# Kernel optimization log

Measured on AMD Instinct MI355X. Metric: run time of the kernel, lower is better.

Reference implementation:

```python
import jax, jax.numpy as jnp
from jax import lax
import numpy as np

VOCAB = 100
EMBED = 16
STATE = 7
OUT = 10
B, T = 4096, 512


def setup_inputs() -> dict:
    key = jax.random.key(0)
    k0, k1, k2, k3, k4 = jax.random.split(key, 5)
    tokens = jax.random.randint(k0, (B, T), 0, VOCAB, dtype=jnp.int32)
    emb = jax.random.normal(k1, (VOCAB, EMBED), dtype=jnp.float32) * 0.05
    # LSTMCell params, Keras gate order: i, f, g(candidate), o
    W = jax.random.normal(k2, (EMBED, 4 * STATE), dtype=jnp.float32) * 0.1
    U = jax.random.normal(k3, (STATE, 4 * STATE), dtype=jnp.float32) * 0.1
    # unit_forget_bias=True in Keras: forget-gate bias initialized to 1
    b = jnp.concatenate([jnp.zeros(STATE), jnp.ones(STATE), jnp.zeros(2 * STATE)]).astype(jnp.float32)
    Wd = jax.random.normal(k4, (STATE, OUT), dtype=jnp.float32) * 0.1
    bd = jnp.zeros((OUT,), dtype=jnp.float32)
    return {"tokens": tokens, "emb": emb, "W": W, "U": U, "b": b, "Wd": Wd, "bd": bd}


def reference(tokens, emb, W, U, b, Wd, bd):
    x = emb[tokens]                      # [B, T, E] embedding lookup
    x_tm = jnp.swapaxes(x, 0, 1)         # [T, B, E] time-major for scan

    def step(carry, xt):
        h, c = carry                     # [B, S] each
        z = xt @ W + h @ U + b           # [B, 4S]
        zi, zf, zg, zo = jnp.split(z, 4, axis=-1)
        i = jax.nn.sigmoid(zi)
        f = jax.nn.sigmoid(zf)
        g = jnp.tanh(zg)
        o = jax.nn.sigmoid(zo)
        c_new = f * c + i * g
        h_new = o * jnp.tanh(c_new)
        return (h_new, c_new), h_new

    h0 = jnp.zeros((tokens.shape[0], STATE), dtype=x.dtype)
    c0 = jnp.zeros_like(h0)
    _, hs = lax.scan(step, (h0, c0), x_tm)   # hs: [T, B, S]
    h_seq = jnp.swapaxes(hs, 0, 1)           # [B, T, S]
    logits = h_seq @ Wd + bd                 # [B, T, 10]
    return jax.nn.softmax(logits, axis=-1)
```

## Files before the change

kernel.cpp:

```cpp
#include <hip/hip_runtime.h>

#define VOCABN 100
#define EMBEDN 16
#define STATEN 7
#define OUTN   10
#define BATCHN 4096
#define SEQT   512
#define L2E 1.44269504088896340736f

__device__ __forceinline__ float fexp2(float x){ float r; asm("v_exp_f32 %0, %1":"=v"(r):"v"(x)); return r; }
__device__ __forceinline__ float frcp (float x){ float r; asm("v_rcp_f32 %0, %1":"=v"(r):"v"(x)); return r; }

template<int C> __device__ __forceinline__ int dppi(int x){
  return __builtin_amdgcn_update_dpp(0, x, C, 0xF, 0xF, true);
}
template<int C> __device__ __forceinline__ float dppf(float x){
  return __int_as_float(__builtin_amdgcn_update_dpp(0, __float_as_int(x), C, 0xF, 0xF, true));
}

__global__ void embw_kernel(const float* __restrict__ emb, const float* __restrict__ W,
                            const float* __restrict__ b, float* __restrict__ embw){
  int v = blockIdx.x, j = threadIdx.x;
  int pos = j >> 1, g2 = j & 1;
  int s = pos >> 1, p = pos & 1, gate = p*2 + g2;
  float val = 0.0f;
  if (s < STATEN) {
    int col = gate*STATEN + s;
    val = b[col];
    #pragma unroll
    for (int e = 0; e < EMBEDN; ++e) val = fmaf(emb[v*EMBEDN+e], W[e*28+col], val);
    val *= (gate == 2) ? (2.0f*L2E) : (-L2E);
  }
  embw[v*32 + pos*2 + g2] = val;
}

__global__ void __launch_bounds__(64,1)
lstm_kernel(const int* __restrict__ tokens, const float* __restrict__ embw,
            const float* __restrict__ U, const float* __restrict__ Wd,
            const float* __restrict__ bdv, float* __restrict__ out){
  __shared__ float embW_s[VOCABN*32];
  __shared__ int   tok_s[4*520];

  const int L = threadIdx.x;
  const int b0 = blockIdx.x*4;

  for (int i=L;i<VOCABN*8;i+=64) ((float4*)embW_s)[i]=((const float4*)embw)[i];
  for (int i=L;i<512;i+=64){ int r=i>>7,c4=i&127;
    int4 v=((const int4*)(tokens+(size_t)(b0+r)*SEQT))[c4];
    *((int4*)&tok_s[r*520+c4*4])=v; }
  if (L<4){ tok_s[L*520+512]=0; tok_s[L*520+513]=0; tok_s[L*520+514]=0; }
  __syncthreads();

  const int pos=L&15, ch=L>>4, s=pos>>1, p=pos&1;

  int sg[8];
  sg[0]=s;
  sg[1]=dppi<0x122>(s); sg[2]=dppi<0x124>(s); sg[3]=dppi<0x126>(s);
  sg[4]=dppi<0x128>(s); sg[5]=dppi<0x12A>(s); sg[6]=dppi<0x12C>(s); sg[7]=dppi<0x12E>(s);

  float Uc0[8], Uc1[8];
  {
    const int gA=p*2, gB=p*2+1;
    const float sA = (gA==2)?(2.0f*L2E):(-L2E);
    const float sB = (gB==2)?(2.0f*L2E):(-L2E);
    #pragma unroll
    for (int k=0;k<8;++k){
      int sk=sg[k]; bool vld=(sk<STATEN)&&(s<STATEN);
      Uc0[k]= vld ? U[sk*28+gA*7+s]*sA : 0.0f;
      Uc1[k]= vld ? U[sk*28+gB*7+s]*sB : 0.0f;
    }
  }
  float Wdc[8][5], bdr[5];
  #pragma unroll
  for (int k=0;k<8;++k){ int sk=sg[k];
    #pragma unroll
    for (int o=0;o<5;++o) Wdc[k][o] = (sk<STATEN)? Wd[sk*10+p*5+o]*L2E : 0.0f; }
  #pragma unroll
  for (int o=0;o<5;++o) bdr[o]=bdv[p*5+o]*L2E;

  const int* trow=&tok_s[ch*520];
  float* outp = out + ((size_t)(b0+ch)*SEQT + s)*OUTN + p*5;

  float hh[8], hc[8], lg[5], ee[5];
  #pragma unroll
  for (int k=0;k<8;++k){ hh[k]=0.0f; hc[k]=0.0f; }
  #pragma unroll
  for (int o=0;o<5;++o){ lg[o]=0.0f; ee[o]=0.0f; }
  float mx=0.0f, rs=0.0f;

  int tk2 = trow[2];
  float2 pf0 = *(const float2*)&embW_s[trow[0]*32+pos*2];
  float2 pf1 = *(const float2*)&embW_s[trow[1]*32+pos*2];
  float Cc=0.0f, h=0.0f;

  for (int t8=0;t8<SEQT;t8+=8){
    #pragma unroll
    for (int u=0;u<8;++u){
      float2 pf2 = *(const float2*)&embW_s[tk2*32+pos*2];
      int tk3 = trow[t8+u+3];

      float r0=h;
      float r1=dppf<0x122>(h), r2=dppf<0x124>(h), r3=dppf<0x126>(h);
      float r4=dppf<0x128>(h), r5=dppf<0x12A>(h), r6=dppf<0x12C>(h), r7=dppf<0x12E>(h);

      bool cap = (s==((u+7)&7));
      hh[0]=cap?r0:hh[0]; hh[1]=cap?r1:hh[1]; hh[2]=cap?r2:hh[2]; hh[3]=cap?r3:hh[3];
      hh[4]=cap?r4:hh[4]; hh[5]=cap?r5:hh[5]; hh[6]=cap?r6:hh[6]; hh[7]=cap?r7:hh[7];

      if (u==0){ hc[0]=hh[0];hc[1]=hh[1];hc[2]=hh[2];hc[3]=hh[3];
                 hc[4]=hh[4];hc[5]=hh[5];hc[6]=hh[6];hc[7]=hh[7]; }
      if (u==1){
        float a0=bdr[0], a1=bdr[1];
        #pragma unroll
        for (int k=0;k<8;++k){ a0=__builtin_fmaf(hc[k],Wdc[k][0],a0);
                               a1=__builtin_fmaf(hc[k],Wdc[k][1],a1); }
        lg[0]=a0; lg[1]=a1; }
      if (u==2){
        float a2=bdr[2], a3=bdr[3];
        #pragma unroll
        for (int k=0;k<8;++k){ a2=__builtin_fmaf(hc[k],Wdc[k][2],a2);
                               a3=__builtin_fmaf(hc[k],Wdc[k][3],a3); }
        lg[2]=a2; lg[3]=a3; }
      if (u==3){
        float a4=bdr[4];
        #pragma unroll
        for (int k=0;k<8;++k) a4=__builtin_fmaf(hc[k],Wdc[k][4],a4);
        lg[4]=a4; }
      if (u==4){
        float m=fmaxf(fmaxf(fmaxf(lg[0],lg[1]),fmaxf(lg[2],lg[3])),lg[4]);
        mx=fmaxf(m, dppf<0xB1>(m)); }
      if (u==5){
        ee[0]=fexp2(lg[0]-mx); ee[1]=fexp2(lg[1]-mx); ee[2]=fexp2(lg[2]-mx);
        ee[3]=fexp2(lg[3]-mx); ee[4]=fexp2(lg[4]-mx); }
      if (u==6){
        float sm=((ee[0]+ee[1])+(ee[2]+ee[3]))+ee[4];
        rs=frcp(sm + dppf<0xB1>(sm)); }
      if (u==7){
        if (t8>0){
          outp[0]=ee[0]*rs; outp[1]=ee[1]*rs; outp[2]=ee[2]*rs;
          outp[3]=ee[3]*rs; outp[4]=ee[4]*rs;
          outp += 8*OUTN;
        } }

      float zA, zB;
      { float q0=__builtin_fmaf(r0,Uc0[0],pf0.x);
        float q1=__builtin_fmaf(r1,Uc0[1], r2*Uc0[2]);
        float q2=__builtin_fmaf(r3,Uc0[3], r4*Uc0[4]);
        float q3=__builtin_fmaf(r5,Uc0[5], r6*Uc0[6]);
        zA=(q0+q1)+((q2+q3)+r7*Uc0[7]); }
      { float q0=__builtin_fmaf(r0,Uc1[0],pf0.y);
        float q1=__builtin_fmaf(r1,Uc1[1], r2*Uc1[2]);
        float q2=__builtin_fmaf(r3,Uc1[3], r4*Uc1[4]);
        float q3=__builtin_fmaf(r5,Uc1[5], r6*Uc1[6]);
        zB=(q0+q1)+((q2+q3)+r7*Uc1[7]); }

      float gA=frcp(1.0f+fexp2(zA));
      float gB=frcp(1.0f+fexp2(zB));
      float gg_s=__builtin_fmaf(gA,-4.0f*L2E,2.0f*L2E);
      float gg_x=dppf<0xB1>(gg_s);
      float go_x=dppf<0xB1>(gB);
      Cc=__builtin_fmaf(gB,Cc,gA*gg_x);
      float rcpC=frcp(1.0f+fexp2(Cc));
      float rcpC_x=dppf<0xB1>(rcpC);
      float go_u = p ? gB     : go_x;
      float rc_u = p ? rcpC_x : rcpC;
      h = __builtin_fmaf(-2.0f*go_u, rc_u, go_u);

      pf0=pf1; pf1=pf2; tk2=tk3;
    }
  }

  {
    float r0=h;
    float r1=dppf<0x122>(h), r2=dppf<0x124>(h), r3=dppf<0x126>(h);
    float r4=dppf<0x128>(h), r5=dppf<0x12A>(h), r6=dppf<0x12C>(h), r7=dppf<0x12E>(h);
    bool cap = (s==7);
    hh[0]=cap?r0:hh[0]; hh[1]=cap?r1:hh[1]; hh[2]=cap?r2:hh[2]; hh[3]=cap?r3:hh[3];
    hh[4]=cap?r4:hh[4]; hh[5]=cap?r5:hh[5]; hh[6]=cap?r6:hh[6]; hh[7]=cap?r7:hh[7];
    float a[5];
    #pragma unroll
    for (int o=0;o<5;++o){ a[o]=bdr[o];
      #pragma unroll
      for (int k=0;k<8;++k) a[o]=__builtin_fmaf(hh[k],Wdc[k][o],a[o]); }
    float m=fmaxf(fmaxf(fmaxf(a[0],a[1]),fmaxf(a[2],a[3])),a[4]);
    m=fmaxf(m, dppf<0xB1>(m));
    float e0=fexp2(a[0]-m), e1=fexp2(a[1]-m), e2=fexp2(a[2]-m),
          e3=fexp2(a[3]-m), e4=fexp2(a[4]-m);
    float sm=((e0+e1)+(e2+e3))+e4;
    float r=frcp(sm + dppf<0xB1>(sm));
    outp[0]=e0*r; outp[1]=e1*r; outp[2]=e2*r; outp[3]=e3*r; outp[4]=e4*r;
  }
}

extern "C" void kernel_launch(void* const* d_in, const int* in_sizes, int n_in,
                              void* d_out, int out_size, void* d_ws, size_t ws_size,
                              hipStream_t stream) {
  const int*   tokens = (const int*)d_in[0];
  const float* emb    = (const float*)d_in[1];
  const float* W      = (const float*)d_in[2];
  const float* U      = (const float*)d_in[3];
  const float* b      = (const float*)d_in[4];
  const float* Wd     = (const float*)d_in[5];
  const float* bd     = (const float*)d_in[6];
  float* outp = (float*)d_out;
  float* embw = (float*)d_ws;

  embw_kernel<<<dim3(VOCABN), dim3(32), 0, stream>>>(emb, W, b, embw);
  lstm_kernel<<<dim3(BATCHN/4), dim3(64), 0, stream>>>(tokens, embw, U, Wd, bd, outp);
}
```

Measured before the change: 88.30 us.

## Split LSTM recurrence and softmax output into producer/consumer wavefronts

The block grows to 128 threads covering 8 sequences. One wavefront runs two independent recurrence chains (A and B) interleaved to hide latency, using packed v2f FMAs for the gate pre-activations. It writes each step's h into a double-buffered shared-memory ring. A second wavefront reads the ring after a per-8-step barrier and computes the dense layer and softmax, replacing the per-step staggered output work. This takes the output projection off the serial recurrence path, at the cost of a block barrier every 8 steps and half as many blocks.

```diff
diff --git a/kernel.cpp b/kernel.cpp
--- a/kernel.cpp
+++ b/kernel.cpp
@@ -7,6 +7,8 @@
 #define BATCHN 4096
 #define SEQT   512
 #define L2E 1.44269504088896340736f
+
+typedef float v2f __attribute__((ext_vector_type(2)));
 
 __device__ __forceinline__ float fexp2(float x){ float r; asm("v_exp_f32 %0, %1":"=v"(r):"v"(x)); return r; }
 __device__ __forceinline__ float frcp (float x){ float r; asm("v_rcp_f32 %0, %1":"=v"(r):"v"(x)); return r; }
@@ -34,128 +36,57 @@
   embw[v*32 + pos*2 + g2] = val;
 }
 
-__global__ void __launch_bounds__(64,1)
+__global__ void __launch_bounds__(128)
 lstm_kernel(const int* __restrict__ tokens, const float* __restrict__ embw,
             const float* __restrict__ U, const float* __restrict__ Wd,
             const float* __restrict__ bdv, float* __restrict__ out){
   __shared__ float embW_s[VOCABN*32];
-  __shared__ int   tok_s[4*520];
+  __shared__ int   tok_s[8*520];
+  __shared__ float hring[2*8*8*16];
 
-  const int L = threadIdx.x;
-  const int b0 = blockIdx.x*4;
+  const int tid = threadIdx.x;
+  const int b0 = blockIdx.x*8;
 
-  for (int i=L;i<VOCABN*8;i+=64) ((float4*)embW_s)[i]=((const float4*)embw)[i];
-  for (int i=L;i<512;i+=64){ int r=i>>7,c4=i&127;
+  for (int i=tid;i<VOCABN*8;i+=128) ((float4*)embW_s)[i]=((const float4*)embw)[i];
+  for (int i=tid;i<8*128;i+=128){ int r=i>>7,c4=i&127;
     int4 v=((const int4*)(tokens+(size_t)(b0+r)*SEQT))[c4];
     *((int4*)&tok_s[r*520+c4*4])=v; }
-  if (L<4){ tok_s[L*520+512]=0; tok_s[L*520+513]=0; tok_s[L*520+514]=0; }
+  if (tid<8){ tok_s[tid*520+512]=0; tok_s[tid*520+513]=0; tok_s[tid*520+514]=0; }
   __syncthreads();
 
-  const int pos=L&15, ch=L>>4, s=pos>>1, p=pos&1;
+  if (tid < 64) {
+    const int pos=tid&15, g=tid>>4, s=pos>>1, p=pos&1;
 
-  int sg[8];
-  sg[0]=s;
-  sg[1]=dppi<0x122>(s); sg[2]=dppi<0x124>(s); sg[3]=dppi<0x126>(s);
-  sg[4]=dppi<0x128>(s); sg[5]=dppi<0x12A>(s); sg[6]=dppi<0x12C>(s); sg[7]=dppi<0x12E>(s);
+    int sg[8];
+    sg[0]=s;
+    sg[1]=dppi<0x122>(s); sg[2]=dppi<0x124>(s); sg[3]=dppi<0x126>(s);
+    sg[4]=dppi<0x128>(s); sg[5]=dppi<0x12A>(s); sg[6]=dppi<0x12C>(s); sg[7]=dppi<0x12E>(s);
 
-  float Uc0[8], Uc1[8];
-  {
-    const int gA=p*2, gB=p*2+1;
-    const float sA = (gA==2)?(2.0f*L2E):(-L2E);
-    const float sB = (gB==2)?(2.0f*L2E):(-L2E);
-    #pragma unroll
-    for (int k=0;k<8;++k){
-      int sk=sg[k]; bool vld=(sk<STATEN)&&(s<STATEN);
-      Uc0[k]= vld ? U[sk*28+gA*7+s]*sA : 0.0f;
-      Uc1[k]= vld ? U[sk*28+gB*7+s]*sB : 0.0f;
+    v2f Ucp[8];
+    {
+      const int gA=p*2, gB=p*2+1;
+      const float sA = (gA==2)?(2.0f*L2E):(-L2E);
+      const float sB = (gB==2)?(2.0f*L2E):(-L2E);
+      #pragma unroll
+      for (int k=0;k<8;++k){
+        int sk=sg[k]; bool vld=(sk<STATEN)&&(s<STATEN);
+        Ucp[k].x = vld ? U[sk*28+gA*7+s]*sA : 0.0f;
+        Ucp[k].y = vld ? U[sk*28+gB*7+s]*sB : 0.0f;
+      }
     }
-  }
-  float Wdc[8][5], bdr[5];
-  #pragma unroll
-  for (int k=0;k<8;++k){ int sk=sg[k];
-    #pragma unroll
-    for (int o=0;o<5;++o) Wdc[k][o] = (sk<STATEN)? Wd[sk*10+p*5+o]*L2E : 0.0f; }
-  #pragma unroll
-  for (int o=0;o<5;++o) bdr[o]=bdv[p*5+o]*L2E;
 
-  const int* trow=&tok_s[ch*520];
-  float* outp = out + ((size_t)(b0+ch)*SEQT + s)*OUTN + p*5;
-
-  float hh[8], hc[8], lg[5], ee[5];
-  #pragma unroll
-  for (int k=0;k<8;++k){ hh[k]=0.0f; hc[k]=0.0f; }
-  #pragma unroll
-  for (int o=0;o<5;++o){ lg[o]=0.0f; ee[o]=0.0f; }
-  float mx=0.0f, rs=0.0f;
-
-  int tk2 = trow[2];
-  float2 pf0 = *(const float2*)&embW_s[trow[0]*32+pos*2];
-  float2 pf1 = *(const float2*)&embW_s[trow[1]*32+pos*2];
-  float Cc=0.0f, h=0.0f;
-
-  for (int t8=0;t8<SEQT;t8+=8){
-    #pragma unroll
-    for (int u=0;u<8;++u){
-      float2 pf2 = *(const float2*)&embW_s[tk2*32+pos*2];
-      int tk3 = trow[t8+u+3];
-
+    auto STEP=[&](float& h, float& Cc, const v2f& pf0){
       float r0=h;
       float r1=dppf<0x122>(h), r2=dppf<0x124>(h), r3=dppf<0x126>(h);
       float r4=dppf<0x128>(h), r5=dppf<0x12A>(h), r6=dppf<0x12C>(h), r7=dppf<0x12E>(h);
-
-      bool cap = (s==((u+7)&7));
-      hh[0]=cap?r0:hh[0]; hh[1]=cap?r1:hh[1]; hh[2]=cap?r2:hh[2]; hh[3]=cap?r3:hh[3];
-      hh[4]=cap?r4:hh[4]; hh[5]=cap?r5:hh[5]; hh[6]=cap?r6:hh[6]; hh[7]=cap?r7:hh[7];
-
-      if (u==0){ hc[0]=hh[0];hc[1]=hh[1];hc[2]=hh[2];hc[3]=hh[3];
-                 hc[4]=hh[4];hc[5]=hh[5];hc[6]=hh[6];hc[7]=hh[7]; }
-      if (u==1){
-        float a0=bdr[0], a1=bdr[1];
-        #pragma unroll
-        for (int k=0;k<8;++k){ a0=__builtin_fmaf(hc[k],Wdc[k][0],a0);
-                               a1=__builtin_fmaf(hc[k],Wdc[k][1],a1); }
-        lg[0]=a0; lg[1]=a1; }
-      if (u==2){
-        float a2=bdr[2], a3=bdr[3];
-        #pragma unroll
-        for (int k=0;k<8;++k){ a2=__builtin_fmaf(hc[k],Wdc[k][2],a2);
-                               a3=__builtin_fmaf(hc[k],Wdc[k][3],a3); }
-        lg[2]=a2; lg[3]=a3; }
-      if (u==3){
-        float a4=bdr[4];
-        #pragma unroll
-        for (int k=0;k<8;++k) a4=__builtin_fmaf(hc[k],Wdc[k][4],a4);
-        lg[4]=a4; }
-      if (u==4){
-        float m=fmaxf(fmaxf(fmaxf(lg[0],lg[1]),fmaxf(lg[2],lg[3])),lg[4]);
-        mx=fmaxf(m, dppf<0xB1>(m)); }
-      if (u==5){
-        ee[0]=fexp2(lg[0]-mx); ee[1]=fexp2(lg[1]-mx); ee[2]=fexp2(lg[2]-mx);
-        ee[3]=fexp2(lg[3]-mx); ee[4]=fexp2(lg[4]-mx); }
-      if (u==6){
-        float sm=((ee[0]+ee[1])+(ee[2]+ee[3]))+ee[4];
-        rs=frcp(sm + dppf<0xB1>(sm)); }
-      if (u==7){
-        if (t8>0){
-          outp[0]=ee[0]*rs; outp[1]=ee[1]*rs; outp[2]=ee[2]*rs;
-          outp[3]=ee[3]*rs; outp[4]=ee[4]*rs;
-          outp += 8*OUTN;
-        } }
-
-      float zA, zB;
-      { float q0=__builtin_fmaf(r0,Uc0[0],pf0.x);
-        float q1=__builtin_fmaf(r1,Uc0[1], r2*Uc0[2]);
-        float q2=__builtin_fmaf(r3,Uc0[3], r4*Uc0[4]);
-        float q3=__builtin_fmaf(r5,Uc0[5], r6*Uc0[6]);
-        zA=(q0+q1)+((q2+q3)+r7*Uc0[7]); }
-      { float q0=__builtin_fmaf(r0,Uc1[0],pf0.y);
-        float q1=__builtin_fmaf(r1,Uc1[1], r2*Uc1[2]);
-        float q2=__builtin_fmaf(r3,Uc1[3], r4*Uc1[4]);
-        float q3=__builtin_fmaf(r5,Uc1[5], r6*Uc1[6]);
-        zB=(q0+q1)+((q2+q3)+r7*Uc1[7]); }
-
-      float gA=frcp(1.0f+fexp2(zA));
-      float gB=frcp(1.0f+fexp2(zB));
+      v2f z01=__builtin_elementwise_fma((v2f){r1,r1},Ucp[1],
+              __builtin_elementwise_fma((v2f){r0,r0},Ucp[0],pf0));
+      v2f z23=__builtin_elementwise_fma((v2f){r3,r3},Ucp[3],(v2f){r2,r2}*Ucp[2]);
+      v2f z45=__builtin_elementwise_fma((v2f){r5,r5},Ucp[5],(v2f){r4,r4}*Ucp[4]);
+      v2f z67=__builtin_elementwise_fma((v2f){r7,r7},Ucp[7],(v2f){r6,r6}*Ucp[6]);
+      v2f zv=(z01+z23)+(z45+z67);
+      float gA=frcp(1.0f+fexp2(zv.x));
+      float gB=frcp(1.0f+fexp2(zv.y));
       float gg_s=__builtin_fmaf(gA,-4.0f*L2E,2.0f*L2E);
       float gg_x=dppf<0xB1>(gg_s);
       float go_x=dppf<0xB1>(gB);
@@ -164,31 +95,82 @@
       float rcpC_x=dppf<0xB1>(rcpC);
       float go_u = p ? gB     : go_x;
       float rc_u = p ? rcpC_x : rcpC;
-      h = __builtin_fmaf(-2.0f*go_u, rc_u, go_u);
+      h=__builtin_fmaf(-2.0f*go_u, rc_u, go_u);
+    };
 
-      pf0=pf1; pf1=pf2; tk2=tk3;
+    const int* trA=&tok_s[g*520];
+    const int* trB=&tok_s[(g+4)*520];
+
+    int tkA2=trA[2], tkB2=trB[2];
+    v2f pfA0=*(const v2f*)&embW_s[trA[0]*32+pos*2];
+    v2f pfA1=*(const v2f*)&embW_s[trA[1]*32+pos*2];
+    v2f pfB0=*(const v2f*)&embW_s[trB[0]*32+pos*2];
+    v2f pfB1=*(const v2f*)&embW_s[trB[1]*32+pos*2];
+    float CcA=0.0f,hA=0.0f,CcB=0.0f,hB=0.0f;
+
+    for (int m=0;m<64;++m){
+      float* hslot=&hring[(m&1)*1024];
+      #pragma unroll
+      for (int u=0;u<8;++u){
+        const int t=m*8+u;
+        v2f pfA2=*(const v2f*)&embW_s[tkA2*32+pos*2];
+        v2f pfB2=*(const v2f*)&embW_s[tkB2*32+pos*2];
+        int tkA3=trA[t+3], tkB3=trB[t+3];
+
+        STEP(hA,CcA,pfA0);
+        STEP(hB,CcB,pfB0);
+        hslot[u*128 + g*16 + pos]=hA;
+        hslot[u*128 + (g+4)*16 + pos]=hB;
+
+        pfA0=pfA1; pfA1=pfA2; tkA2=tkA3;
+        pfB0=pfB1; pfB1=pfB2; tkB2=tkB3;
+      }
+      __syncthreads();
     }
-  }
+  } else {
+    const int lq=tid-64, ch=lq>>3, tq=lq&7;
 
-  {
-    float r0=h;
-    float r1=dppf<0x122>(h), r2=dppf<0x124>(h), r3=dppf<0x126>(h);
-    float r4=dppf<0x128>(h), r5=dppf<0x12A>(h), r6=dppf<0x12C>(h), r7=dppf<0x12E>(h);
-    bool cap = (s==7);
-    hh[0]=cap?r0:hh[0]; hh[1]=cap?r1:hh[1]; hh[2]=cap?r2:hh[2]; hh[3]=cap?r3:hh[3];
-    hh[4]=cap?r4:hh[4]; hh[5]=cap?r5:hh[5]; hh[6]=cap?r6:hh[6]; hh[7]=cap?r7:hh[7];
-    float a[5];
+    float Wdc[7][10], bdr[10];
     #pragma unroll
-    for (int o=0;o<5;++o){ a[o]=bdr[o];
+    for (int s2=0;s2<7;++s2)
       #pragma unroll
-      for (int k=0;k<8;++k) a[o]=__builtin_fmaf(hh[k],Wdc[k][o],a[o]); }
-    float m=fmaxf(fmaxf(fmaxf(a[0],a[1]),fmaxf(a[2],a[3])),a[4]);
-    m=fmaxf(m, dppf<0xB1>(m));
-    float e0=fexp2(a[0]-m), e1=fexp2(a[1]-m), e2=fexp2(a[2]-m),
-          e3=fexp2(a[3]-m), e4=fexp2(a[4]-m);
-    float sm=((e0+e1)+(e2+e3))+e4;
-    float r=frcp(sm + dppf<0xB1>(sm));
-    outp[0]=e0*r; outp[1]=e1*r; outp[2]=e2*r; outp[3]=e3*r; outp[4]=e4*r;
+      for (int o=0;o<OUTN;++o) Wdc[s2][o]=Wd[s2*10+o]*L2E;
+    #pragma unroll
+    for (int o=0;o<OUTN;++o) bdr[o]=bdv[o]*L2E;
+
+    float* outp = out + ((size_t)(b0+ch)*SEQT + tq)*OUTN;
+
+    for (int m=0;m<64;++m){
+      __syncthreads();
+      const float* hp=&hring[(m&1)*1024 + tq*128 + ch*16];
+      float h0=hp[0], h1=hp[2], h2=hp[4], h3=hp[6];
+      float h4=hp[8], h5=hp[10], h6=hp[12];
+
+      float lg[10];
+      #pragma unroll
+      for (int o=0;o<OUTN;++o){
+        float a=bdr[o];
+        a=__builtin_fmaf(h0,Wdc[0][o],a); a=__builtin_fmaf(h1,Wdc[1][o],a);
+        a=__builtin_fmaf(h2,Wdc[2][o],a); a=__builtin_fmaf(h3,Wdc[3][o],a);
+        a=__builtin_fmaf(h4,Wdc[4][o],a); a=__builtin_fmaf(h5,Wdc[5][o],a);
+        a=__builtin_fmaf(h6,Wdc[6][o],a);
+        lg[o]=a;
+      }
+      float mx=lg[0];
+      #pragma unroll
+      for (int o=1;o<OUTN;++o) mx=fmaxf(mx,lg[o]);
+      float e[10], sm=0.0f;
+      #pragma unroll
+      for (int o=0;o<OUTN;++o){ e[o]=fexp2(lg[o]-mx); sm+=e[o]; }
+      float rs=frcp(sm);
+      float2* op=(float2*)outp;
+      op[0]=make_float2(e[0]*rs,e[1]*rs);
+      op[1]=make_float2(e[2]*rs,e[3]*rs);
+      op[2]=make_float2(e[4]*rs,e[5]*rs);
+      op[3]=make_float2(e[6]*rs,e[7]*rs);
+      op[4]=make_float2(e[8]*rs,e[9]*rs);
+      outp += 8*OUTN;
+    }
   }
 }
 
@@ -206,5 +188,5 @@
   float* embw = (float*)d_ws;
 
   embw_kernel<<<dim3(VOCABN), dim3(32), 0, stream>>>(emb, W, b, embw);
-  lstm_kernel<<<dim3(BATCHN/4), dim3(64), 0, stream>>>(tokens, embw, U, Wd, bd, outp);
+  lstm_kernel<<<dim3(BATCHN/8), dim3(128), 0, stream>>>(tokens, embw, U, Wd, bd, outp);
 }
```

Measured after the change: 125.8 us. 1.42x slower.

## Halve sequences per wave and pack gate dot products into v2f FMAs

Applied to the files above, without the earlier changes.

Each 64-lane block now handles 2 batch sequences instead of 4. Lanes 32-63 duplicate the work of lanes 0-31 and are masked off for stores, and twice as many blocks are launched. The occupancy hint of one block per CU is dropped. The recurrent U-matrix dot products for the two gates are rewritten with 2-wide vector FMAs so they can map to packed FP32 instructions. This trades half the useful lanes per wave for more waves to hide the serial per-step latency, which doubles the total instruction work.

```diff
diff --git a/kernel.cpp b/kernel.cpp
--- a/kernel.cpp
+++ b/kernel.cpp
@@ -7,6 +7,8 @@
 #define BATCHN 4096
 #define SEQT   512
 #define L2E 1.44269504088896340736f
+
+typedef float v2f __attribute__((ext_vector_type(2)));
 
 __device__ __forceinline__ float fexp2(float x){ float r; asm("v_exp_f32 %0, %1":"=v"(r):"v"(x)); return r; }
 __device__ __forceinline__ float frcp (float x){ float r; asm("v_rcp_f32 %0, %1":"=v"(r):"v"(x)); return r; }
@@ -34,31 +36,33 @@
   embw[v*32 + pos*2 + g2] = val;
 }
 
-__global__ void __launch_bounds__(64,1)
+__global__ void __launch_bounds__(64)
 lstm_kernel(const int* __restrict__ tokens, const float* __restrict__ embw,
             const float* __restrict__ U, const float* __restrict__ Wd,
             const float* __restrict__ bdv, float* __restrict__ out){
   __shared__ float embW_s[VOCABN*32];
-  __shared__ int   tok_s[4*520];
-
-  const int L = threadIdx.x;
-  const int b0 = blockIdx.x*4;
-
-  for (int i=L;i<VOCABN*8;i+=64) ((float4*)embW_s)[i]=((const float4*)embw)[i];
-  for (int i=L;i<512;i+=64){ int r=i>>7,c4=i&127;
+  __shared__ int   tok_s[2*520];
+
+  const int tid = threadIdx.x;
+  const int b0 = blockIdx.x*2;
+
+  for (int i=tid;i<VOCABN*8;i+=64) ((float4*)embW_s)[i]=((const float4*)embw)[i];
+  for (int i=tid;i<2*128;i+=64){ int r=i>>7,c4=i&127;
     int4 v=((const int4*)(tokens+(size_t)(b0+r)*SEQT))[c4];
     *((int4*)&tok_s[r*520+c4*4])=v; }
-  if (L<4){ tok_s[L*520+512]=0; tok_s[L*520+513]=0; tok_s[L*520+514]=0; }
+  if (tid<2){ tok_s[tid*520+512]=0; tok_s[tid*520+513]=0; tok_s[tid*520+514]=0; }
   __syncthreads();
 
-  const int pos=L&15, ch=L>>4, s=pos>>1, p=pos&1;
+  const int pos=tid&15, g=tid>>4, s=pos>>1, p=pos&1;
+  const int ch=g&1;
+  const bool act=(g<2);
 
   int sg[8];
   sg[0]=s;
   sg[1]=dppi<0x122>(s); sg[2]=dppi<0x124>(s); sg[3]=dppi<0x126>(s);
   sg[4]=dppi<0x128>(s); sg[5]=dppi<0x12A>(s); sg[6]=dppi<0x12C>(s); sg[7]=dppi<0x12E>(s);
 
-  float Uc0[8], Uc1[8];
+  v2f Ucp[8];
   {
     const int gA=p*2, gB=p*2+1;
     const float sA = (gA==2)?(2.0f*L2E):(-L2E);
@@ -66,8 +70,8 @@
     #pragma unroll
     for (int k=0;k<8;++k){
       int sk=sg[k]; bool vld=(sk<STATEN)&&(s<STATEN);
-      Uc0[k]= vld ? U[sk*28+gA*7+s]*sA : 0.0f;
-      Uc1[k]= vld ? U[sk*28+gB*7+s]*sB : 0.0f;
+      Ucp[k].x = vld ? U[sk*28+gA*7+s]*sA : 0.0f;
+      Ucp[k].y = vld ? U[sk*28+gB*7+s]*sB : 0.0f;
     }
   }
   float Wdc[8][5], bdr[5];
@@ -89,14 +93,14 @@
   float mx=0.0f, rs=0.0f;
 
   int tk2 = trow[2];
-  float2 pf0 = *(const float2*)&embW_s[trow[0]*32+pos*2];
-  float2 pf1 = *(const float2*)&embW_s[trow[1]*32+pos*2];
+  v2f pf0 = *(const v2f*)&embW_s[trow[0]*32+pos*2];
+  v2f pf1 = *(const v2f*)&embW_s[trow[1]*32+pos*2];
   float Cc=0.0f, h=0.0f;
 
   for (int t8=0;t8<SEQT;t8+=8){
     #pragma unroll
     for (int u=0;u<8;++u){
-      float2 pf2 = *(const float2*)&embW_s[tk2*32+pos*2];
+      v2f pf2 = *(const v2f*)&embW_s[tk2*32+pos*2];
       int tk3 = trow[t8+u+3];
 
       float r0=h;
@@ -136,26 +140,22 @@
         float sm=((ee[0]+ee[1])+(ee[2]+ee[3]))+ee[4];
         rs=frcp(sm + dppf<0xB1>(sm)); }
       if (u==7){
-        if (t8>0){
+        if (t8>0 && act){
           outp[0]=ee[0]*rs; outp[1]=ee[1]*rs; outp[2]=ee[2]*rs;
           outp[3]=ee[3]*rs; outp[4]=ee[4]*rs;
-          outp += 8*OUTN;
-        } }
-
-      float zA, zB;
-      { float q0=__builtin_fmaf(r0,Uc0[0],pf0.x);
-        float q1=__builtin_fmaf(r1,Uc0[1], r2*Uc0[2]);
-        float q2=__builtin_fmaf(r3,Uc0[3], r4*Uc0[4]);
-        float q3=__builtin_fmaf(r5,Uc0[5], r6*Uc0[6]);
-        zA=(q0+q1)+((q2+q3)+r7*Uc0[7]); }
-      { float q0=__builtin_fmaf(r0,Uc1[0],pf0.y);
-        float q1=__builtin_fmaf(r1,Uc1[1], r2*Uc1[2]);
-        float q2=__builtin_fmaf(r3,Uc1[3], r4*Uc1[4]);
-        float q3=__builtin_fmaf(r5,Uc1[5], r6*Uc1[6]);
-        zB=(q0+q1)+((q2+q3)+r7*Uc1[7]); }
-
-      float gA=frcp(1.0f+fexp2(zA));
-      float gB=frcp(1.0f+fexp2(zB));
+        }
+        if (t8>0) outp += 8*OUTN;
+      }
+
+      v2f z01=__builtin_elementwise_fma((v2f){r1,r1},Ucp[1],
+              __builtin_elementwise_fma((v2f){r0,r0},Ucp[0],pf0));
+      v2f z23=__builtin_elementwise_fma((v2f){r3,r3},Ucp[3],(v2f){r2,r2}*Ucp[2]);
+      v2f z45=__builtin_elementwise_fma((v2f){r5,r5},Ucp[5],(v2f){r4,r4}*Ucp[4]);
+      v2f z67=__builtin_elementwise_fma((v2f){r7,r7},Ucp[7],(v2f){r6,r6}*Ucp[6]);
+      v2f zv=(z01+z23)+(z45+z67);
+
+      float gA=frcp(1.0f+fexp2(zv.x));
+      float gB=frcp(1.0f+fexp2(zv.y));
       float gg_s=__builtin_fmaf(gA,-4.0f*L2E,2.0f*L2E);
       float gg_x=dppf<0xB1>(gg_s);
       float go_x=dppf<0xB1>(gB);
@@ -164,7 +164,7 @@
       float rcpC_x=dppf<0xB1>(rcpC);
       float go_u = p ? gB     : go_x;
       float rc_u = p ? rcpC_x : rcpC;
-      h = __builtin_fmaf(-2.0f*go_u, rc_u, go_u);
+      h=__builtin_fmaf(-2.0f*go_u, rc_u, go_u);
 
       pf0=pf1; pf1=pf2; tk2=tk3;
     }
@@ -188,7 +188,9 @@
           e3=fexp2(a[3]-m), e4=fexp2(a[4]-m);
     float sm=((e0+e1)+(e2+e3))+e4;
     float r=frcp(sm + dppf<0xB1>(sm));
-    outp[0]=e0*r; outp[1]=e1*r; outp[2]=e2*r; outp[3]=e3*r; outp[4]=e4*r;
+    if (act){
+      outp[0]=e0*r; outp[1]=e1*r; outp[2]=e2*r; outp[3]=e3*r; outp[4]=e4*r;
+    }
   }
 }
 
@@ -206,5 +208,5 @@
   float* embw = (float*)d_ws;
 
   embw_kernel<<<dim3(VOCABN), dim3(32), 0, stream>>>(emb, W, b, embw);
-  lstm_kernel<<<dim3(BATCHN/4), dim3(64), 0, stream>>>(tokens, embw, U, Wd, bd, outp);
-}
+  lstm_kernel<<<dim3(BATCHN/2), dim3(64), 0, stream>>>(tokens, embw, U, Wd, bd, outp);
+}
```

Measured after the change: 133.4 us. 51.1% more time.

## Pack 8 sequences per wave with one lane per state, packed-FP32 gates, rational tanh

Applied to the files above, without the earlier changes.

Each lane now computes all four gates for its state unit, where before two lanes shared them. This doubles the number of batch rows per 64-lane block (8 instead of 4) and halves the grid. The gate pre-activations use v2f packed FMAs, and sigmoid/tanh are replaced by a clamped Padé rational tanh approximation (sigmoid expressed through tanh), which removes the DPP lane exchanges inside the recurrence. The embedding-projection table is stored with a per-token rotated slot so that float4 LDS reads avoid bank conflicts. The risks are a longer per-lane dependency chain, more registers (Wdc is now 8x10) and a small accuracy loss from the tanh approximation clamped at ±4.5.

```diff
diff --git a/kernel.cpp b/kernel.cpp
--- a/kernel.cpp
+++ b/kernel.cpp
@@ -8,6 +8,8 @@
 #define SEQT   512
 #define L2E 1.44269504088896340736f
 
+typedef float v2f __attribute__((ext_vector_type(2)));
+
 __device__ __forceinline__ float fexp2(float x){ float r; asm("v_exp_f32 %0, %1":"=v"(r):"v"(x)); return r; }
 __device__ __forceinline__ float frcp (float x){ float r; asm("v_rcp_f32 %0, %1":"=v"(r):"v"(x)); return r; }
 
@@ -16,22 +18,45 @@
 }
 template<int C> __device__ __forceinline__ float dppf(float x){
   return __int_as_float(__builtin_amdgcn_update_dpp(0, __float_as_int(x), C, 0xF, 0xF, true));
+}
+
+__device__ __forceinline__ v2f ptanh2(v2f z){
+  v2f t = __builtin_elementwise_min(
+            __builtin_elementwise_max(z, (v2f){-4.5f,-4.5f}), (v2f){4.5f,4.5f});
+  v2f u = t*t;
+  v2f n = __builtin_elementwise_fma(
+            __builtin_elementwise_fma(u + (v2f){378.0f,378.0f}, u,
+                                      (v2f){17325.0f,17325.0f}), u,
+            (v2f){135135.0f,135135.0f});
+  v2f d = __builtin_elementwise_fma(
+            __builtin_elementwise_fma(
+              __builtin_elementwise_fma(u,(v2f){28.0f,28.0f},(v2f){3150.0f,3150.0f}),
+              u, (v2f){62370.0f,62370.0f}), u,
+            (v2f){135135.0f,135135.0f});
+  v2f nt = n*t;
+  return (v2f){ nt.x*frcp(d.x), nt.y*frcp(d.y) };
+}
+__device__ __forceinline__ float ptanh1(float z){
+  float t = fminf(fmaxf(z,-4.5f),4.5f);
+  float u = t*t;
+  float n = __builtin_fmaf(__builtin_fmaf(u+378.0f,u,17325.0f),u,135135.0f);
+  float d = __builtin_fmaf(__builtin_fmaf(__builtin_fmaf(u,28.0f,3150.0f),u,62370.0f),u,135135.0f);
+  return (n*t)*frcp(d);
 }
 
 __global__ void embw_kernel(const float* __restrict__ emb, const float* __restrict__ W,
                             const float* __restrict__ b, float* __restrict__ embw){
   int v = blockIdx.x, j = threadIdx.x;
-  int pos = j >> 1, g2 = j & 1;
-  int s = pos >> 1, p = pos & 1, gate = p*2 + g2;
+  int s = j >> 2, gate = j & 3;
   float val = 0.0f;
   if (s < STATEN) {
     int col = gate*STATEN + s;
     val = b[col];
     #pragma unroll
     for (int e = 0; e < EMBEDN; ++e) val = fmaf(emb[v*EMBEDN+e], W[e*28+col], val);
-    val *= (gate == 2) ? (2.0f*L2E) : (-L2E);
-  }
-  embw[v*32 + pos*2 + g2] = val;
+    val *= (gate == 2) ? 1.0f : 0.5f;
+  }
+  embw[v*32 + ((s+v)&7)*4 + gate] = val;
 }
 
 __global__ void __launch_bounds__(64,1)
@@ -39,64 +64,62 @@
             const float* __restrict__ U, const float* __restrict__ Wd,
             const float* __restrict__ bdv, float* __restrict__ out){
   __shared__ float embW_s[VOCABN*32];
-  __shared__ int   tok_s[4*520];
-
-  const int L = threadIdx.x;
-  const int b0 = blockIdx.x*4;
-
-  for (int i=L;i<VOCABN*8;i+=64) ((float4*)embW_s)[i]=((const float4*)embw)[i];
-  for (int i=L;i<512;i+=64){ int r=i>>7,c4=i&127;
+  __shared__ int   tok_s[8*520];
+
+  const int tid = threadIdx.x;
+  const int b0 = blockIdx.x*8;
+
+  for (int i=tid;i<VOCABN*8;i+=64) ((float4*)embW_s)[i]=((const float4*)embw)[i];
+  for (int i=tid;i<8*128;i+=64){ int r=i>>7,c4=i&127;
     int4 v=((const int4*)(tokens+(size_t)(b0+r)*SEQT))[c4];
     *((int4*)&tok_s[r*520+c4*4])=v; }
-  if (L<4){ tok_s[L*520+512]=0; tok_s[L*520+513]=0; tok_s[L*520+514]=0; }
+  if (tid<8){ tok_s[tid*520+512]=0; tok_s[tid*520+513]=0; tok_s[tid*520+514]=0; }
   __syncthreads();
 
-  const int pos=L&15, ch=L>>4, s=pos>>1, p=pos&1;
+  const int pos=tid&15, row=tid>>4, s=pos>>1, q=pos&1;
+  const int ch = row*2 + q;
 
   int sg[8];
   sg[0]=s;
   sg[1]=dppi<0x122>(s); sg[2]=dppi<0x124>(s); sg[3]=dppi<0x126>(s);
   sg[4]=dppi<0x128>(s); sg[5]=dppi<0x12A>(s); sg[6]=dppi<0x12C>(s); sg[7]=dppi<0x12E>(s);
 
-  float Uc0[8], Uc1[8];
-  {
-    const int gA=p*2, gB=p*2+1;
-    const float sA = (gA==2)?(2.0f*L2E):(-L2E);
-    const float sB = (gB==2)?(2.0f*L2E):(-L2E);
-    #pragma unroll
-    for (int k=0;k<8;++k){
-      int sk=sg[k]; bool vld=(sk<STATEN)&&(s<STATEN);
-      Uc0[k]= vld ? U[sk*28+gA*7+s]*sA : 0.0f;
-      Uc1[k]= vld ? U[sk*28+gB*7+s]*sB : 0.0f;
-    }
-  }
-  float Wdc[8][5], bdr[5];
+  v2f Uif[8], Ugo[8];
+  #pragma unroll
+  for (int k=0;k<8;++k){
+    int sk=sg[k]; bool vld=(sk<STATEN)&&(s<STATEN);
+    Uif[k].x = vld ? U[sk*28 + 0*7 + s]*0.5f : 0.0f;
+    Uif[k].y = vld ? U[sk*28 + 1*7 + s]*0.5f : 0.0f;
+    Ugo[k].x = vld ? U[sk*28 + 2*7 + s]      : 0.0f;
+    Ugo[k].y = vld ? U[sk*28 + 3*7 + s]*0.5f : 0.0f;
+  }
+  float Wdc[8][10], bdr[10];
   #pragma unroll
   for (int k=0;k<8;++k){ int sk=sg[k];
     #pragma unroll
-    for (int o=0;o<5;++o) Wdc[k][o] = (sk<STATEN)? Wd[sk*10+p*5+o]*L2E : 0.0f; }
-  #pragma unroll
-  for (int o=0;o<5;++o) bdr[o]=bdv[p*5+o]*L2E;
+    for (int o=0;o<OUTN;++o) Wdc[k][o] = (sk<STATEN)? Wd[sk*10+o]*L2E : 0.0f; }
+  #pragma unroll
+  for (int o=0;o<OUTN;++o) bdr[o]=bdv[o]*L2E;
 
   const int* trow=&tok_s[ch*520];
-  float* outp = out + ((size_t)(b0+ch)*SEQT + s)*OUTN + p*5;
-
-  float hh[8], hc[8], lg[5], ee[5];
+  float* outp = out + ((size_t)(b0+ch)*SEQT + s)*OUTN;
+
+  float hh[8], hc[8], lg[10], ee[10];
   #pragma unroll
   for (int k=0;k<8;++k){ hh[k]=0.0f; hc[k]=0.0f; }
   #pragma unroll
-  for (int o=0;o<5;++o){ lg[o]=0.0f; ee[o]=0.0f; }
+  for (int o=0;o<OUTN;++o){ lg[o]=0.0f; ee[o]=0.0f; }
   float mx=0.0f, rs=0.0f;
 
   int tk2 = trow[2];
-  float2 pf0 = *(const float2*)&embW_s[trow[0]*32+pos*2];
-  float2 pf1 = *(const float2*)&embW_s[trow[1]*32+pos*2];
+  float4 pf0 = *(const float4*)&embW_s[trow[0]*32 + (((s+trow[0])&7)<<2)];
+  float4 pf1 = *(const float4*)&embW_s[trow[1]*32 + (((s+trow[1])&7)<<2)];
   float Cc=0.0f, h=0.0f;
 
   for (int t8=0;t8<SEQT;t8+=8){
     #pragma unroll
     for (int u=0;u<8;++u){
-      float2 pf2 = *(const float2*)&embW_s[tk2*32+pos*2];
+      float4 pf2 = *(const float4*)&embW_s[tk2*32 + (((s+tk2)&7)<<2)];
       int tk3 = trow[t8+u+3];
 
       float r0=h;
@@ -110,61 +133,68 @@
       if (u==0){ hc[0]=hh[0];hc[1]=hh[1];hc[2]=hh[2];hc[3]=hh[3];
                  hc[4]=hh[4];hc[5]=hh[5];hc[6]=hh[6];hc[7]=hh[7]; }
       if (u==1){
-        float a0=bdr[0], a1=bdr[1];
         #pragma unroll
-        for (int k=0;k<8;++k){ a0=__builtin_fmaf(hc[k],Wdc[k][0],a0);
-                               a1=__builtin_fmaf(hc[k],Wdc[k][1],a1); }
-        lg[0]=a0; lg[1]=a1; }
+        for (int o=0;o<3;++o){ float a=bdr[o];
+          #pragma unroll
+          for (int k=0;k<8;++k) a=__builtin_fmaf(hc[k],Wdc[k][o],a);
+          lg[o]=a; } }
       if (u==2){
-        float a2=bdr[2], a3=bdr[3];
         #pragma unroll
-        for (int k=0;k<8;++k){ a2=__builtin_fmaf(hc[k],Wdc[k][2],a2);
-                               a3=__builtin_fmaf(hc[k],Wdc[k][3],a3); }
-        lg[2]=a2; lg[3]=a3; }
+        for (int o=3;o<6;++o){ float a=bdr[o];
+          #pragma unroll
+          for (int k=0;k<8;++k) a=__builtin_fmaf(hc[k],Wdc[k][o],a);
+          lg[o]=a; } }
       if (u==3){
-        float a4=bdr[4];
         #pragma unroll
-        for (int k=0;k<8;++k) a4=__builtin_fmaf(hc[k],Wdc[k][4],a4);
-        lg[4]=a4; }
+        for (int o=6;o<OUTN;++o){ float a=bdr[o];
+          #pragma unroll
+          for (int k=0;k<8;++k) a=__builtin_fmaf(hc[k],Wdc[k][o],a);
+          lg[o]=a; } }
       if (u==4){
-        float m=fmaxf(fmaxf(fmaxf(lg[0],lg[1]),fmaxf(lg[2],lg[3])),lg[4]);
-        mx=fmaxf(m, dppf<0xB1>(m)); }
+        float m0=fmaxf(fmaxf(lg[0],lg[1]),fmaxf(lg[2],lg[3]));
+        float m1=fmaxf(fmaxf(lg[4],lg[5]),fmaxf(lg[6],lg[7]));
+        mx=fmaxf(fmaxf(m0,m1),fmaxf(lg[8],lg[9])); }
       if (u==5){
         ee[0]=fexp2(lg[0]-mx); ee[1]=fexp2(lg[1]-mx); ee[2]=fexp2(lg[2]-mx);
-        ee[3]=fexp2(lg[3]-mx); ee[4]=fexp2(lg[4]-mx); }
+        ee[3]=fexp2(lg[3]-mx); ee[4]=fexp2(lg[4]-mx); ee[5]=fexp2(lg[5]-mx);
+        ee[6]=fexp2(lg[6]-mx); ee[7]=fexp2(lg[7]-mx); ee[8]=fexp2(lg[8]-mx);
+        ee[9]=fexp2(lg[9]-mx); }
       if (u==6){
-        float sm=((ee[0]+ee[1])+(ee[2]+ee[3]))+ee[4];
-        rs=frcp(sm + dppf<0xB1>(sm)); }
+        float sm=(((ee[0]+ee[1])+(ee[2]+ee[3]))+((ee[4]+ee[5])+(ee[6]+ee[7])))+(ee[8]+ee[9]);
+        rs=frcp(sm); }
       if (u==7){
         if (t8>0){
-          outp[0]=ee[0]*rs; outp[1]=ee[1]*rs; outp[2]=ee[2]*rs;
-          outp[3]=ee[3]*rs; outp[4]=ee[4]*rs;
+          float2* op=(float2*)outp;
+          op[0]=make_float2(ee[0]*rs,ee[1]*rs);
+          op[1]=make_float2(ee[2]*rs,ee[3]*rs);
+          op[2]=make_float2(ee[4]*rs,ee[5]*rs);
+          op[3]=make_float2(ee[6]*rs,ee[7]*rs);
+          op[4]=make_float2(ee[8]*rs,ee[9]*rs);
           outp += 8*OUTN;
         } }
 
-      float zA, zB;
-      { float q0=__builtin_fmaf(r0,Uc0[0],pf0.x);
-        float q1=__builtin_fmaf(r1,Uc0[1], r2*Uc0[2]);
-        float q2=__builtin_fmaf(r3,Uc0[3], r4*Uc0[4]);
-        float q3=__builtin_fmaf(r5,Uc0[5], r6*Uc0[6]);
-        zA=(q0+q1)+((q2+q3)+r7*Uc0[7]); }
-      { float q0=__builtin_fmaf(r0,Uc1[0],pf0.y);
-        float q1=__builtin_fmaf(r1,Uc1[1], r2*Uc1[2]);
-        float q2=__builtin_fmaf(r3,Uc1[3], r4*Uc1[4]);
-        float q3=__builtin_fmaf(r5,Uc1[5], r6*Uc1[6]);
-        zB=(q0+q1)+((q2+q3)+r7*Uc1[7]); }
-
-      float gA=frcp(1.0f+fexp2(zA));
-      float gB=frcp(1.0f+fexp2(zB));
-      float gg_s=__builtin_fmaf(gA,-4.0f*L2E,2.0f*L2E);
-      float gg_x=dppf<0xB1>(gg_s);
-      float go_x=dppf<0xB1>(gB);
-      Cc=__builtin_fmaf(gB,Cc,gA*gg_x);
-      float rcpC=frcp(1.0f+fexp2(Cc));
-      float rcpC_x=dppf<0xB1>(rcpC);
-      float go_u = p ? gB     : go_x;
-      float rc_u = p ? rcpC_x : rcpC;
-      h = __builtin_fmaf(-2.0f*go_u, rc_u, go_u);
+      v2f zif = {pf0.x, pf0.y}, zgo = {pf0.z, pf0.w};
+      v2f a01 = __builtin_elementwise_fma((v2f){r1,r1},Uif[1],
+                __builtin_elementwise_fma((v2f){r0,r0},Uif[0],zif));
+      v2f a23 = __builtin_elementwise_fma((v2f){r3,r3},Uif[3],(v2f){r2,r2}*Uif[2]);
+      v2f a45 = __builtin_elementwise_fma((v2f){r5,r5},Uif[5],(v2f){r4,r4}*Uif[4]);
+      v2f a67 = __builtin_elementwise_fma((v2f){r7,r7},Uif[7],(v2f){r6,r6}*Uif[6]);
+      zif = (a01+a23)+(a45+a67);
+      v2f b01 = __builtin_elementwise_fma((v2f){r1,r1},Ugo[1],
+                __builtin_elementwise_fma((v2f){r0,r0},Ugo[0],zgo));
+      v2f b23 = __builtin_elementwise_fma((v2f){r3,r3},Ugo[3],(v2f){r2,r2}*Ugo[2]);
+      v2f b45 = __builtin_elementwise_fma((v2f){r5,r5},Ugo[5],(v2f){r4,r4}*Ugo[4]);
+      v2f b67 = __builtin_elementwise_fma((v2f){r7,r7},Ugo[7],(v2f){r6,r6}*Ugo[6]);
+      zgo = (b01+b23)+(b45+b67);
+
+      v2f tif = ptanh2(zif);
+      v2f tgo = ptanh2(zgo);
+      float gi = __builtin_fmaf(tif.x,0.5f,0.5f);
+      float gf = __builtin_fmaf(tif.y,0.5f,0.5f);
+      float gg = tgo.x;
+      float go = __builtin_fmaf(tgo.y,0.5f,0.5f);
+      Cc = __builtin_fmaf(gf,Cc,gi*gg);
+      h  = go * ptanh1(Cc);
 
       pf0=pf1; pf1=pf2; tk2=tk3;
     }
@@ -177,18 +207,24 @@
     bool cap = (s==7);
     hh[0]=cap?r0:hh[0]; hh[1]=cap?r1:hh[1]; hh[2]=cap?r2:hh[2]; hh[3]=cap?r3:hh[3];
     hh[4]=cap?r4:hh[4]; hh[5]=cap?r5:hh[5]; hh[6]=cap?r6:hh[6]; hh[7]=cap?r7:hh[7];
-    float a[5];
-    #pragma unroll
-    for (int o=0;o<5;++o){ a[o]=bdr[o];
+    float a[10];
+    #pragma unroll
+    for (int o=0;o<OUTN;++o){ a[o]=bdr[o];
       #pragma unroll
       for (int k=0;k<8;++k) a[o]=__builtin_fmaf(hh[k],Wdc[k][o],a[o]); }
-    float m=fmaxf(fmaxf(fmaxf(a[0],a[1]),fmaxf(a[2],a[3])),a[4]);
-    m=fmaxf(m, dppf<0xB1>(m));
-    float e0=fexp2(a[0]-m), e1=fexp2(a[1]-m), e2=fexp2(a[2]-m),
-          e3=fexp2(a[3]-m), e4=fexp2(a[4]-m);
-    float sm=((e0+e1)+(e2+e3))+e4;
-    float r=frcp(sm + dppf<0xB1>(sm));
-    outp[0]=e0*r; outp[1]=e1*r; outp[2]=e2*r; outp[3]=e3*r; outp[4]=e4*r;
+    float m0=fmaxf(fmaxf(a[0],a[1]),fmaxf(a[2],a[3]));
+    float m1=fmaxf(fmaxf(a[4],a[5]),fmaxf(a[6],a[7]));
+    float m=fmaxf(fmaxf(m0,m1),fmaxf(a[8],a[9]));
+    float e[10], sm=0.0f;
+    #pragma unroll
+    for (int o=0;o<OUTN;++o){ e[o]=fexp2(a[o]-m); sm+=e[o]; }
+    float r=frcp(sm);
+    float2* op=(float2*)outp;
+    op[0]=make_float2(e[0]*r,e[1]*r);
+    op[1]=make_float2(e[2]*r,e[3]*r);
+    op[2]=make_float2(e[4]*r,e[5]*r);
+    op[3]=make_float2(e[6]*r,e[7]*r);
+    op[4]=make_float2(e[8]*r,e[9]*r);
   }
 }
 
@@ -206,5 +242,5 @@
   float* embw = (float*)d_ws;
 
   embw_kernel<<<dim3(VOCABN), dim3(32), 0, stream>>>(emb, W, b, embw);
-  lstm_kernel<<<dim3(BATCHN/4), dim3(64), 0, stream>>>(tokens, embw, U, Wd, bd, outp);
-}
+  lstm_kernel<<<dim3(BATCHN/8), dim3(64), 0, stream>>>(tokens, embw, U, Wd, bd, outp);
+}
```

New measurement: 134.8 us. 52.6% more time.
